# Kernel tuning notes

Measured on AMD Instinct MI355X. Metric: run time of the kernel, lower is better.

The kernel has to match this reference:

```python
import jax, jax.numpy as jnp
import numpy as np

# static config (matches init_kwargs and spatial_shapes input)
SPATIAL = ((100, 100), (50, 50), (25, 25), (13, 13))  # (H, W) per level
D_MODEL, N_HEADS, N_LEVELS, N_POINTS, D_FFN = 256, 8, 4, 4, 1024
D_HEAD = D_MODEL // N_HEADS
LEN_IN = sum(h * w for h, w in SPATIAL)
LEVEL_START = np.cumsum([0] + [h * w for h, w in SPATIAL])[:-1]


def setup_inputs() -> dict:
    key = jax.random.key(0)
    ks = jax.random.split(key, 12)
    N = 2
    f = lambda k, shape, s=0.02: jax.random.normal(k, shape, jnp.float32) * s
    return {
        "src": jax.random.normal(ks[0], (N, LEN_IN, D_MODEL), jnp.float32),
        "pos": jax.random.normal(ks[1], (N, LEN_IN, D_MODEL), jnp.float32),
        "reference_points": jax.random.uniform(ks[2], (N, LEN_IN, N_LEVELS, 2), jnp.float32),
        "spatial_shapes": jnp.asarray(SPATIAL, jnp.int32),
        "level_start_index": jnp.asarray(LEVEL_START, jnp.int32),
        "W_value": f(ks[3], (D_MODEL, D_MODEL)),
        "b_value": jnp.zeros((D_MODEL,), jnp.float32),
        "W_off": f(ks[4], (D_MODEL, N_HEADS * N_LEVELS * N_POINTS * 2)),
        "b_off": f(ks[5], (N_HEADS * N_LEVELS * N_POINTS * 2,), 0.5),
        "W_attn": f(ks[6], (D_MODEL, N_HEADS * N_LEVELS * N_POINTS)),
        "b_attn": jnp.zeros((N_HEADS * N_LEVELS * N_POINTS,), jnp.float32),
        "W_out": f(ks[7], (D_MODEL, D_MODEL)),
        "b_out": jnp.zeros((D_MODEL,), jnp.float32),
        "W1": f(ks[8], (D_MODEL, D_FFN)),
        "b1": jnp.zeros((D_FFN,), jnp.float32),
        "W2": f(ks[9], (D_FFN, D_MODEL)),
        "b2": jnp.zeros((D_MODEL,), jnp.float32),
        "g1": jnp.ones((D_MODEL,), jnp.float32),
        "be1": jnp.zeros((D_MODEL,), jnp.float32),
        "g2": jnp.ones((D_MODEL,), jnp.float32),
        "be2": jnp.zeros((D_MODEL,), jnp.float32),
    }


def _ln(x, g, b, eps=1e-5):
    mu = x.mean(-1, keepdims=True)
    var = ((x - mu) ** 2).mean(-1, keepdims=True)
    return (x - mu) * jax.lax.rsqrt(var + eps) * g + b


def _bilinear(v, loc, H, W):
    # v: [N, heads, H*W, Dh]; loc: [N, Lq, heads, P, 2] normalized to [0,1]
    # replicates F.grid_sample(align_corners=False, padding_mode='zeros') with grid=2*loc-1
    N, Lq, Hh, P, _ = loc.shape
    x = loc[..., 0] * W - 0.5
    y = loc[..., 1] * H - 0.5
    x0 = jnp.floor(x)
    y0 = jnp.floor(y)
    wx1 = x - x0
    wy1 = y - y0
    x0i = x0.astype(jnp.int32)
    y0i = y0.astype(jnp.int32)
    out = jnp.zeros((N, Lq, Hh, P, v.shape[-1]), v.dtype)
    for dy, dx in ((0, 0), (0, 1), (1, 0), (1, 1)):
        xi = x0i + dx
        yi = y0i + dy
        w = (wx1 if dx else 1.0 - wx1) * (wy1 if dy else 1.0 - wy1)
        valid = (xi >= 0) & (xi < W) & (yi >= 0) & (yi < H)
        idx = jnp.clip(yi, 0, H - 1) * W + jnp.clip(xi, 0, W - 1)  # [N,Lq,Hh,P]
        idx = idx.transpose(0, 2, 1, 3).reshape(N, Hh, Lq * P)
        g = jax.vmap(jax.vmap(lambda vm, im: vm[im]))(v, idx)  # [N,Hh,Lq*P,Dh]
        g = g.reshape(N, Hh, Lq, P, -1).transpose(0, 2, 1, 3, 4)
        out = out + (w * valid)[..., None] * g
    return out


def reference(src, pos, reference_points, spatial_shapes, level_start_index,
              W_value, b_value, W_off, b_off, W_attn, b_attn, W_out, b_out,
              W1, b1, W2, b2, g1, be1, g2, be2):
    N, Lq, _ = src.shape
    value = (src @ W_value + b_value).reshape(N, Lq, N_HEADS, D_HEAD)
    q = src + pos  # with_pos_embed
    off = (q @ W_off + b_off).reshape(N, Lq, N_HEADS, N_LEVELS, N_POINTS, 2)
    attn = (q @ W_attn + b_attn).reshape(N, Lq, N_HEADS, N_LEVELS * N_POINTS)
    attn = jax.nn.softmax(attn, axis=-1).reshape(N, Lq, N_HEADS, N_LEVELS, N_POINTS)
    # offset_normalizer = (W, H) per level
    normalizer = jnp.asarray([[w, h] for h, w in SPATIAL], jnp.float32)
    loc = reference_points[:, :, None, :, None, :] + off / normalizer[None, None, None, :, None, :]
    out = jnp.zeros((N, Lq, N_HEADS, D_HEAD), jnp.float32)
    for l, (H, W) in enumerate(SPATIAL):
        s = int(LEVEL_START[l])
        v_l = value[:, s:s + H * W].transpose(0, 2, 1, 3)  # [N, heads, H*W, Dh]
        samp = _bilinear(v_l, loc[:, :, :, l], H, W)       # [N, Lq, heads, P, Dh]
        out = out + jnp.einsum('nqhp,nqhpc->nqhc', attn[:, :, :, l], samp)
    src2 = out.reshape(N, Lq, D_MODEL) @ W_out + b_out
    x = _ln(src + src2, g1, be1)
    ffn = jax.nn.relu(x @ W1 + b1) @ W2 + b2
    return _ln(x + ffn, g2, be2)
```

## Files before the change

### kernel.cpp

```cpp
#include <hip/hip_runtime.h>
#include <hip/hip_bf16.h>
#include <cstdint>

#define D_MODEL   256
#define N_HEADS   8
#define N_LEVELS  4
#define N_POINTS  4
#define D_FFN     1024
#define D_HEAD    32
#define LEN_IN    13294
#define NBATCH    2
#define M_TOK     (NBATCH * LEN_IN)
#define M_PAD     26624

__constant__ int c_lvl_h[4] = {100, 50, 25, 13};
__constant__ int c_lvl_w[4] = {100, 50, 25, 13};
__constant__ int c_lvl_s[4] = {0, 10000, 12500, 13125};

typedef __attribute__((ext_vector_type(8))) __bf16 bf16x8;
typedef __attribute__((ext_vector_type(4))) __bf16 bf16x4;
typedef __attribute__((ext_vector_type(4))) float  f32x4;
typedef __attribute__((ext_vector_type(4))) uint32_t u32x4;

__device__ __forceinline__ float bflo(uint32_t w) { return __uint_as_float(w << 16); }
__device__ __forceinline__ float bfhi(uint32_t w) { return __uint_as_float(w & 0xffff0000u); }

__device__ __forceinline__ void lds_direct16(const void* g, void* l) {
    __builtin_amdgcn_global_load_lds(
        (const __attribute__((address_space(1))) uint32_t*)(uintptr_t)g,
        (__attribute__((address_space(3))) uint32_t*)(uintptr_t)l,
        16, 0, 0);
}

__global__ __launch_bounds__(256) void prep(
    const float* __restrict__ s0, const float* __restrict__ s1, const float* __restrict__ s2,
    const float* __restrict__ s3, const float* __restrict__ s4, const float* __restrict__ s5,
    __bf16* __restrict__ d0, __bf16* __restrict__ d1, __bf16* __restrict__ d2,
    __bf16* __restrict__ d3, __bf16* __restrict__ d4, __bf16* __restrict__ d5,
    const float* __restrict__ b_off, const float* __restrict__ b_attn,
    float* __restrict__ bias_oa,
    const float4* __restrict__ src, const float4* __restrict__ pos,
    bf16x4* __restrict__ sb, bf16x4* __restrict__ qb, int n4)
{
    const int tid = threadIdx.x;
    const int b = blockIdx.x;
    if (b >= 737) {
        const int i = (b - 737) * 256 + tid;
        if (i >= n4) return;
        const float4 s = src[i];
        const float4 p = pos[i];
        bf16x4 sv = { (__bf16)s.x, (__bf16)s.y, (__bf16)s.z, (__bf16)s.w };
        bf16x4 qv = { (__bf16)(s.x + p.x), (__bf16)(s.y + p.y),
                      (__bf16)(s.z + p.z), (__bf16)(s.w + p.w) };
        sb[i] = sv;
        qb[i] = qv;
        return;
    }
    if (b == 736) {
        if (tid < 256) bias_oa[tid] = b_off[tid];
        if (tid < 128) bias_oa[256 + tid] = b_attn[tid];
        return;
    }
    const int tx = tid & 31;
    const int ty = tid >> 5;
    const int starts[7] = {0, 64, 128, 160, 224, 480, 736};
    const int Ks[6] = {256, 256, 256, 256, 256, 1024};
    const int Ns[6] = {256, 256, 128, 256, 1024, 256};
    const float* srcs[6] = {s0, s1, s2, s3, s4, s5};
    __bf16* dsts[6] = {d0, d1, d2, d3, d4, d5};
    int i = 0;
    while (b >= starts[i + 1]) ++i;
    const int t = b - starts[i];
    const int K = Ks[i], N = Ns[i];
    const float* W = srcs[i];
    __bf16* Wt = dsts[i];
    const int ntx = N >> 5;
    const int n0 = (t % ntx) * 32;
    const int k0 = (t / ntx) * 32;

    __shared__ float tl[32][33];
    #pragma unroll
    for (int j = 0; j < 4; ++j)
        tl[ty + j * 8][tx] = W[(size_t)(k0 + ty + j * 8) * N + n0 + tx];
    __syncthreads();
    #pragma unroll
    for (int j = 0; j < 4; ++j)
        Wt[(size_t)(n0 + ty + j * 8) * K + k0 + tx] = (__bf16)tl[tx][ty + j * 8];
}

template <bool RELU, int K, bool HEADMAJOR>
__device__ __forceinline__ void gemm_core(
    const __bf16* __restrict__ A, const __bf16* __restrict__ Bt,
    const float* __restrict__ bias, __bf16* __restrict__ C,
    int M, int N, int bm, int bn)
{
    __shared__ __bf16 smem[17408];
    __bf16* As = smem;
    __bf16* Bs = smem + 8192;

    const int tid  = threadIdx.x;
    const int lane = tid & 63;
    const int wv   = tid >> 6;
    const int wm   = (wv >> 1) * 64;
    const int wn   = (wv & 1) * 64;
    const int srow = lane >> 2;
    const int skc  = (lane & 3) * 8;
    const int fm   = lane & 15;
    const int fko  = (lane >> 4) * 8;

    f32x4 acc[4][4] = {};

    for (int k0 = 0; k0 < K; k0 += 64) {
        #pragma unroll
        for (int p = 0; p < 2; ++p) {
            #pragma unroll
            for (int c = 0; c < 2; ++c) {
                const int r = wv * 32 + c * 16;
                lds_direct16(A  + (size_t)(bm + r + srow) * K + k0 + p * 32 + skc, As + p * 4096 + r * 32);
                lds_direct16(Bt + (size_t)(bn + r + srow) * K + k0 + p * 32 + skc, Bs + p * 4096 + r * 32);
            }
        }
        __syncthreads();

        #pragma unroll
        for (int p = 0; p < 2; ++p) {
            bf16x8 af[4], bfr[4];
            #pragma unroll
            for (int t = 0; t < 4; ++t) {
                af[t]  = *(const bf16x8*)(As + p * 4096 + (wm + t * 16 + fm) * 32 + fko);
                bfr[t] = *(const bf16x8*)(Bs + p * 4096 + (wn + t * 16 + fm) * 32 + fko);
            }
            #pragma unroll
            for (int mt = 0; mt < 4; ++mt)
                #pragma unroll
                for (int nt = 0; nt < 4; ++nt)
                    acc[mt][nt] = __builtin_amdgcn_mfma_f32_16x16x32_bf16(
                        af[mt], bfr[nt], acc[mt][nt], 0, 0, 0);
        }
        __syncthreads();
    }

    const int ecol = lane & 15;
    const int erow = (lane >> 4) * 4;
    #pragma unroll
    for (int nt = 0; nt < 4; ++nt) {
        const int cl = wn + nt * 16 + ecol;
        const float bv = bias[bn + cl];
        #pragma unroll
        for (int mt = 0; mt < 4; ++mt) {
            #pragma unroll
            for (int r = 0; r < 4; ++r) {
                const int rl = wm + mt * 16 + erow + r;
                float v = acc[mt][nt][r] + bv;
                if (RELU) v = fmaxf(v, 0.f);
                smem[rl * 136 + cl] = (__bf16)v;
            }
        }
    }
    __syncthreads();
    #pragma unroll
    for (int rr = 0; rr < 8; ++rr) {
        const int idx = rr * 256 + tid;
        if (HEADMAJOR) {
            const int plane = idx >> 9;
            const int row   = (idx >> 2) & 127;
            const int ch4   = idx & 3;
            if (bm + row < M)
                *(bf16x8*)(C + ((size_t)((bn >> 5) + plane) * M_PAD + (bm + row)) * 32 + ch4 * 8) =
                    *(const bf16x8*)(smem + row * 136 + plane * 32 + ch4 * 8);
        } else {
            const int row = idx >> 4;
            const int ch  = idx & 15;
            if (bm + row < M)
                *(bf16x8*)(C + (size_t)(bm + row) * N + bn + ch * 8) =
                    *(const bf16x8*)(smem + row * 136 + ch * 8);
        }
    }
}

__global__ __launch_bounds__(256) void gemm_front(
    const __bf16* __restrict__ A0, const __bf16* __restrict__ B0,
    const float* __restrict__ bi0, __bf16* __restrict__ C0,
    const __bf16* __restrict__ A1, const __bf16* __restrict__ B1,
    const float* __restrict__ bi1, __bf16* __restrict__ C1, int M)
{
    const int bx = blockIdx.x;
    if (bx < 2)
        gemm_core<false, 256, true>(A0, B0, bi0, C0, M, 256, blockIdx.y * 128, bx * 128);
    else
        gemm_core<false, 256, false>(A1, B1, bi1, C1, M, 384, blockIdx.y * 128, (bx - 2) * 128);
}

__global__ __launch_bounds__(256) void gemm_ffn1(
    const __bf16* __restrict__ A, const __bf16* __restrict__ Bt,
    const float* __restrict__ bias, __bf16* __restrict__ C, int M)
{
    gemm_core<true, 256, false>(A, Bt, bias, C, M, 1024, blockIdx.y * 128, blockIdx.x * 128);
}

template <typename OutT, int K>
__global__ __launch_bounds__(256, 3) void gemm_ln(
    const __bf16* __restrict__ A, const __bf16* __restrict__ Bt,
    const float* __restrict__ bias, const __bf16* __restrict__ res,
    const float* __restrict__ gamma, const float* __restrict__ beta,
    OutT* __restrict__ Cout, int M)
{
    __shared__ __bf16 smem[2][12288];
    __shared__ float lnsum[32][4];
    __shared__ float lnsq[32][4];
    __shared__ float lnstat[32][2];

    const int tid  = threadIdx.x;
    const int lane = tid & 63;
    const int wv   = tid >> 6;
    const int bm   = blockIdx.x * 32;
    const int wn   = wv * 64;
    const int srow = lane >> 2;
    const int skc  = (lane & 3) * 8;
    const int fm   = lane & 15;
    const int fko  = (lane >> 4) * 8;

    f32x4 acc[2][4] = {};

    auto stage = [&](int b, int k0) {
        __bf16* Asw = smem[b] + wv * 1024;
        __bf16* Bsw = smem[b] + 4096;
        lds_direct16(A + (size_t)(bm +  0 + srow) * K + k0 + skc, Asw);
        lds_direct16(A + (size_t)(bm + 16 + srow) * K + k0 + skc, Asw + 512);
        #pragma unroll
        for (int c = 0; c < 4; ++c) {
            const int r = wv * 64 + c * 16;
            lds_direct16(Bt + (size_t)(r + srow) * K + k0 + skc, Bsw + r * 32);
        }
    };
    auto compute = [&](int b) {
        const __bf16* Asw = smem[b] + wv * 1024;
        const __bf16* Bsw = smem[b] + 4096;
        bf16x8 af[2], bfr[4];
        #pragma unroll
        for (int mt = 0; mt < 2; ++mt)
            af[mt] = *(const bf16x8*)(Asw + (mt * 16 + fm) * 32 + fko);
        #pragma unroll
        for (int nt = 0; nt < 4; ++nt)
            bfr[nt] = *(const bf16x8*)(Bsw + (wn + nt * 16 + fm) * 32 + fko);
        #pragma unroll
        for (int mt = 0; mt < 2; ++mt)
            #pragma unroll
            for (int nt = 0; nt < 4; ++nt)
                acc[mt][nt] = __builtin_amdgcn_mfma_f32_16x16x32_bf16(
                    af[mt], bfr[nt], acc[mt][nt], 0, 0, 0);
    };

    stage(0, 0);
    int cur = 0;
    for (int k0 = 32; k0 < K; k0 += 32) {
        stage(cur ^ 1, k0);
        asm volatile("s_waitcnt vmcnt(6)" ::: "memory");
        __builtin_amdgcn_sched_barrier(0);
        compute(cur);
        cur ^= 1;
    }
    asm volatile("s_waitcnt vmcnt(0)" ::: "memory");
    __builtin_amdgcn_sched_barrier(0);
    compute(cur);

    const int ecol = lane & 15;
    const int erow = (lane >> 4) * 4;

    float g4[4], b4[4];
    #pragma unroll
    for (int nt = 0; nt < 4; ++nt) {
        const int col = wn + nt * 16 + ecol;
        g4[nt] = gamma[col];
        b4[nt] = beta[col];
        const float bv = bias[col];
        #pragma unroll
        for (int mt = 0; mt < 2; ++mt) {
            #pragma unroll
            for (int r = 0; r < 4; ++r) {
                const int row = bm + mt * 16 + erow + r;
                acc[mt][nt][r] += bv + (float)res[(size_t)row * 256 + col];
            }
        }
    }

    #pragma unroll
    for (int mt = 0; mt < 2; ++mt) {
        #pragma unroll
        for (int r = 0; r < 4; ++r) {
            float s  = acc[mt][0][r] + acc[mt][1][r] + acc[mt][2][r] + acc[mt][3][r];
            float s2 = acc[mt][0][r] * acc[mt][0][r] + acc[mt][1][r] * acc[mt][1][r]
                     + acc[mt][2][r] * acc[mt][2][r] + acc[mt][3][r] * acc[mt][3][r];
            #pragma unroll
            for (int o = 1; o < 16; o <<= 1) {
                s  += __shfl_xor(s, o);
                s2 += __shfl_xor(s2, o);
            }
            if (ecol == 0) {
                const int rl = mt * 16 + erow + r;
                lnsum[rl][wv] = s;
                lnsq[rl][wv]  = s2;
            }
        }
    }
    __syncthreads();
    if (tid < 32) {
        const float s  = lnsum[tid][0] + lnsum[tid][1] + lnsum[tid][2] + lnsum[tid][3];
        const float s2 = lnsq[tid][0] + lnsq[tid][1] + lnsq[tid][2] + lnsq[tid][3];
        const float mu = s * (1.f / 256.f);
        const float var = s2 * (1.f / 256.f) - mu * mu;
        lnstat[tid][0] = mu;
        lnstat[tid][1] = rsqrtf(var + 1e-5f);
    }
    __syncthreads();

    if constexpr (sizeof(OutT) == 2) {
        __bf16* ct = smem[0];
        #pragma unroll
        for (int mt = 0; mt < 2; ++mt) {
            #pragma unroll
            for (int r = 0; r < 4; ++r) {
                const int rl = mt * 16 + erow + r;
                const float mu = lnstat[rl][0];
                const float rs = lnstat[rl][1];
                #pragma unroll
                for (int nt = 0; nt < 4; ++nt) {
                    const int col = wn + nt * 16 + ecol;
                    ct[rl * 264 + col] = (__bf16)((acc[mt][nt][r] - mu) * rs * g4[nt] + b4[nt]);
                }
            }
        }
        __syncthreads();
        #pragma unroll
        for (int rr = 0; rr < 4; ++rr) {
            const int idx = rr * 256 + tid;
            const int row = idx >> 5;
            const int ch  = idx & 31;
            if (bm + row < M)
                *(bf16x8*)((__bf16*)Cout + (size_t)(bm + row) * 256 + ch * 8) =
                    *(const bf16x8*)(ct + row * 264 + ch * 8);
        }
    } else {
        float* ct = (float*)smem[0];
        #pragma unroll
        for (int hf = 0; hf < 2; ++hf) {
            const int mt = hf;
            #pragma unroll
            for (int r = 0; r < 4; ++r) {
                const int rl   = mt * 16 + erow + r;
                const int rloc = erow + r;
                const float mu = lnstat[rl][0];
                const float rs = lnstat[rl][1];
                #pragma unroll
                for (int nt = 0; nt < 4; ++nt) {
                    const int col = wn + nt * 16 + ecol;
                    ct[rloc * 260 + col] = (acc[mt][nt][r] - mu) * rs * g4[nt] + b4[nt];
                }
            }
            __syncthreads();
            #pragma unroll
            for (int rr = 0; rr < 4; ++rr) {
                const int idx = rr * 256 + tid;
                const int row = idx >> 6;
                const int ch  = idx & 63;
                const int grow = bm + hf * 16 + row;
                if (grow < M) {
                    float4 v = *(const float4*)(ct + row * 260 + ch * 4);
                    *(float4*)((float*)Cout + (size_t)grow * 256 + ch * 4) = v;
                }
            }
            __syncthreads();
        }
    }
}

__global__ __launch_bounds__(256) void msda_sample(
    const __bf16* __restrict__ value,
    const __bf16* __restrict__ oa,
    const float* __restrict__ refp,
    __bf16* __restrict__ out)
{
    __shared__ uint32_t sc[32 * 132];
    __shared__ float sw[32][16];

    const int tid   = threadIdx.x;
    const int blk   = blockIdx.x;
    const int hbase = blockIdx.y * 2;

    if (tid < 32) {
        const int t = tid >> 1;
        const int h = hbase + (tid & 1);
        int row = blk * 16 + t; if (row >= M_TOK) row = M_TOK - 1;
        const __bf16* ap = oa + (size_t)row * 384 + 256 + h * 16;
        const bf16x8 v0 = *(const bf16x8*)ap;
        const bf16x8 v1 = *(const bf16x8*)(ap + 8);
        float e[16];
        #pragma unroll
        for (int i = 0; i < 8; ++i) { e[i] = (float)v0[i]; e[8 + i] = (float)v1[i]; }
        float mx = -1e30f;
        #pragma unroll
        for (int i = 0; i < 16; ++i) mx = fmaxf(mx, e[i]);
        float s = 0.f;
        #pragma unroll
        for (int i = 0; i < 16; ++i) { e[i] = __expf(e[i] - mx); s += e[i]; }
        const float inv = 1.f / s;
        #pragma unroll
        for (int i = 0; i < 16; ++i) sw[tid][i] = e[i] * inv;
    }
    __syncthreads();

    #pragma unroll
    for (int it = 0; it < 2; ++it) {
        const int idx = it * 256 + tid;
        const int t  = idx >> 5;
        const int hl = (idx >> 4) & 1;
        const int lp = idx & 15;
        const int l  = lp >> 2;
        const int h  = hbase + hl;
        int row = blk * 16 + t; if (row >= M_TOK) row = M_TOK - 1;
        const int Ww = c_lvl_w[l];
        const int Hh = c_lvl_h[l];
        const uint32_t opk = *(const uint32_t*)(oa + (size_t)row * 384 + h * 32 + lp * 2);
        const float ox = bflo(opk), oy = bfhi(opk);
        const float rx = refp[((size_t)row * 4 + l) * 2 + 0];
        const float ry = refp[((size_t)row * 4 + l) * 2 + 1];
        const float x = (rx + ox / (float)Ww) * (float)Ww - 0.5f;
        const float y = (ry + oy / (float)Hh) * (float)Hh - 0.5f;
        const float xf = floorf(x), yf = floorf(y);
        const float fx = x - xf,    fy = y - yf;
        const int x0 = (int)xf, y0 = (int)yf;
        const int n  = (row >= LEN_IN) ? 1 : 0;
        const int lvlbase = n * LEN_IN + c_lvl_s[l];
        const float a = sw[t * 2 + hl][lp];
        const int xs = min(max(x0, 0), Ww - 2);
        const int d  = x0 - xs;
        const float wxl = 1.f - fx, wxr = fx;
        const float pw0 = (d == 0) ? wxl : ((d == -1) ? wxr : 0.f);
        const float pw1 = (d == 0) ? wxr : ((d == 1) ? wxl : 0.f);
        uint32_t* p = sc + (t * 2 + hl) * 132 + lp * 8;
        #pragma unroll
        for (int dy = 0; dy < 2; ++dy) {
            const int yi = y0 + dy;
            const int yc = min(max(yi, 0), Hh - 1);
            const bool yv = (yi >= 0) & (yi < Hh);
            const float wy = (dy ? fy : 1.f - fy) * (yv ? a : 0.f);
            const uint32_t boff = (uint32_t)(lvlbase + yc * Ww + xs) * 64u;
            u32x4 pk = { boff, __float_as_uint(pw0 * wy), __float_as_uint(pw1 * wy), 0u };
            *(u32x4*)(p + dy * 4) = pk;
        }
    }
    __syncthreads();

    const int t  = tid >> 4;
    const int hl = (tid >> 3) & 1;
    const int c8 = tid & 7;
    const int h  = hbase + hl;
    const uint32_t* mb = sc + (t * 2 + hl) * 132;
    const char* __restrict__ vpb = (const char*)(value + (size_t)h * (M_PAD * 32));
    const uint32_t lsub = (uint32_t)c8 * 16u;
    const bool hi = (c8 >= 4);
    float acc[8] = {};
    #pragma unroll 8
    for (int qd = 0; qd < 32; ++qd) {
        const u32x4 md = *(const u32x4*)(mb + qd * 4);
        const float w = __uint_as_float(hi ? md.z : md.y);
        const u32x4 v = *(const u32x4*)(vpb + (size_t)(md.x + lsub));
        #pragma unroll
        for (int d2 = 0; d2 < 4; ++d2) {
            acc[2 * d2]     += w * bflo(v[d2]);
            acc[2 * d2 + 1] += w * bfhi(v[d2]);
        }
    }
    #pragma unroll
    for (int j = 0; j < 8; ++j) acc[j] += __shfl_xor(acc[j], 4);
    if (c8 < 4) {
        const int orow = blk * 16 + t;
        if (orow < M_TOK) {
            bf16x8 o;
            #pragma unroll
            for (int j = 0; j < 8; ++j) o[j] = (__bf16)acc[j];
            *(bf16x8*)(out + (size_t)orow * 256 + h * 32 + c8 * 8) = o;
        }
    }
}

extern "C" void kernel_launch(void* const* d_in, const int* in_sizes, int n_in,
                              void* d_out, int out_size, void* d_ws, size_t ws_size,
                              hipStream_t stream)
{
    const float* src     = (const float*)d_in[0];
    const float* pos     = (const float*)d_in[1];
    const float* refp    = (const float*)d_in[2];
    const float* W_value = (const float*)d_in[5];
    const float* b_value = (const float*)d_in[6];
    const float* W_off   = (const float*)d_in[7];
    const float* b_off   = (const float*)d_in[8];
    const float* W_attn  = (const float*)d_in[9];
    const float* b_attn  = (const float*)d_in[10];
    const float* W_out   = (const float*)d_in[11];
    const float* b_out   = (const float*)d_in[12];
    const float* W1      = (const float*)d_in[13];
    const float* b1      = (const float*)d_in[14];
    const float* W2      = (const float*)d_in[15];
    const float* b2      = (const float*)d_in[16];
    const float* g1      = (const float*)d_in[17];
    const float* be1     = (const float*)d_in[18];
    const float* g2      = (const float*)d_in[19];
    const float* be2     = (const float*)d_in[20];
    float* outp = (float*)d_out;

    const int M = M_TOK;
    char* ws = (char*)d_ws;
    const size_t R2 = (size_t)M_PAD * 512;

    __bf16* src_b = (__bf16*)(ws);
    __bf16* q_b   = (__bf16*)(ws + R2);
    __bf16* val_b = (__bf16*)(ws + 2 * R2);
    __bf16* oa    = (__bf16*)(ws + 3 * R2);
    __bf16* samp  = (__bf16*)(ws + 9 * R2 / 2);
    __bf16* x_b   = (__bf16*)(ws + 11 * R2 / 2);
    __bf16* hbuf  = (__bf16*)(ws);
    __bf16* wbase = (__bf16*)(ws + 13 * R2 / 2);
    __bf16* Wt_value = wbase;
    __bf16* Wt_oa    = wbase + 65536;
    __bf16* Wt_out   = wbase + 163840;
    __bf16* Wt1      = wbase + 229376;
    __bf16* Wt2      = wbase + 491520;
    float*  bias_oa  = (float*)(wbase + 753664);

    const dim3 blk(256);
    const int n4 = M * 256 / 4;
    const int gm = M_PAD / 128;

    prep<<<dim3(737 + (n4 + 255) / 256), blk, 0, stream>>>(
        W_value, W_off, W_attn, W_out, W1, W2,
        Wt_value, Wt_oa, Wt_oa + 65536, Wt_out, Wt1, Wt2,
        b_off, b_attn, bias_oa,
        (const float4*)src, (const float4*)pos, (bf16x4*)src_b, (bf16x4*)q_b, n4);

    gemm_front<<<dim3(5, gm), blk, 0, stream>>>(
        src_b, Wt_value, b_value, val_b,
        q_b,   Wt_oa,    bias_oa, oa, M);

    msda_sample<<<dim3((M + 15) / 16, 4), blk, 0, stream>>>(val_b, oa, refp, samp);

    gemm_ln<__bf16, 256><<<dim3(M_PAD / 32), blk, 0, stream>>>(
        samp, Wt_out, b_out, src_b, g1, be1, x_b, M);

    gemm_ffn1<<<dim3(8, gm), blk, 0, stream>>>(x_b, Wt1, b1, hbuf, M);

    gemm_ln<float, 1024><<<dim3(M_PAD / 32), blk, 0, stream>>>(
        hbuf, Wt2, b2, x_b, g2, be2, outp, M);
}
```

Before: 298.2 us.

## Swizzle GEMM block order across XCDs and share A tile in gemm_ln

The front and FFN1 GEMMs now flatten the grid index and remap it so that each XCD (f & 7) handles a contiguous range of M tiles, which should improve L2 reuse of A rows. gemm_ln stops giving each wave its own copy of the A tile and loads a single shared 32x32 A tile, which shrinks shared memory and raises the occupancy hint from 3 to 4 blocks. Synchronisation there changes from per-wave vmcnt waits to block-wide __syncthreads. The risk is that the block barriers and the remap arithmetic add overhead, and the remap assumes a fixed grid shape.

Result: faster. 290.3 us (-2.6%).

```diff
diff --git a/kernel.cpp b/kernel.cpp
--- a/kernel.cpp
+++ b/kernel.cpp
@@ -184,28 +184,38 @@
     const __bf16* __restrict__ A1, const __bf16* __restrict__ B1,
     const float* __restrict__ bi1, __bf16* __restrict__ C1, int M)
 {
-    const int bx = blockIdx.x;
-    if (bx < 2)
-        gemm_core<false, 256, true>(A0, B0, bi0, C0, M, 256, blockIdx.y * 128, bx * 128);
+    const int f   = blockIdx.y * 5 + blockIdx.x;
+    const int xcd = f & 7;
+    const int j   = f >> 3;
+    const int sel = j / 26;
+    const int mm  = j - sel * 26;
+    const int bm  = (xcd * 26 + mm) * 128;
+    if (sel < 2)
+        gemm_core<false, 256, true >(A0, B0, bi0, C0, M, 256, bm, sel * 128);
     else
-        gemm_core<false, 256, false>(A1, B1, bi1, C1, M, 384, blockIdx.y * 128, (bx - 2) * 128);
+        gemm_core<false, 256, false>(A1, B1, bi1, C1, M, 384, bm, (sel - 2) * 128);
 }
 
 __global__ __launch_bounds__(256) void gemm_ffn1(
     const __bf16* __restrict__ A, const __bf16* __restrict__ Bt,
     const float* __restrict__ bias, __bf16* __restrict__ C, int M)
 {
-    gemm_core<true, 256, false>(A, Bt, bias, C, M, 1024, blockIdx.y * 128, blockIdx.x * 128);
+    const int f   = blockIdx.y * 8 + blockIdx.x;
+    const int xcd = f & 7;
+    const int j   = f >> 3;
+    const int nt_ = j / 26;
+    const int mm  = j - nt_ * 26;
+    gemm_core<true, 256, false>(A, Bt, bias, C, M, 1024, (xcd * 26 + mm) * 128, nt_ * 128);
 }
 
 template <typename OutT, int K>
-__global__ __launch_bounds__(256, 3) void gemm_ln(
+__global__ __launch_bounds__(256, 4) void gemm_ln(
     const __bf16* __restrict__ A, const __bf16* __restrict__ Bt,
     const float* __restrict__ bias, const __bf16* __restrict__ res,
     const float* __restrict__ gamma, const float* __restrict__ beta,
     OutT* __restrict__ Cout, int M)
 {
-    __shared__ __bf16 smem[2][12288];
+    __shared__ __bf16 smem[2][9216];
     __shared__ float lnsum[32][4];
     __shared__ float lnsq[32][4];
     __shared__ float lnstat[32][2];
@@ -223,26 +233,27 @@
     f32x4 acc[2][4] = {};
 
     auto stage = [&](int b, int k0) {
-        __bf16* Asw = smem[b] + wv * 1024;
-        __bf16* Bsw = smem[b] + 4096;
-        lds_direct16(A + (size_t)(bm +  0 + srow) * K + k0 + skc, Asw);
-        lds_direct16(A + (size_t)(bm + 16 + srow) * K + k0 + skc, Asw + 512);
+        __bf16* As = smem[b];
+        __bf16* Bs = smem[b] + 1024;
+        if (tid < 128)
+            lds_direct16(A + (size_t)(bm + (tid >> 2)) * K + k0 + (tid & 3) * 8,
+                         As + tid * 8);
         #pragma unroll
         for (int c = 0; c < 4; ++c) {
             const int r = wv * 64 + c * 16;
-            lds_direct16(Bt + (size_t)(r + srow) * K + k0 + skc, Bsw + r * 32);
+            lds_direct16(Bt + (size_t)(r + srow) * K + k0 + skc, Bs + r * 32);
         }
     };
     auto compute = [&](int b) {
-        const __bf16* Asw = smem[b] + wv * 1024;
-        const __bf16* Bsw = smem[b] + 4096;
+        const __bf16* As = smem[b];
+        const __bf16* Bs = smem[b] + 1024;
         bf16x8 af[2], bfr[4];
         #pragma unroll
         for (int mt = 0; mt < 2; ++mt)
-            af[mt] = *(const bf16x8*)(Asw + (mt * 16 + fm) * 32 + fko);
+            af[mt] = *(const bf16x8*)(As + (mt * 16 + fm) * 32 + fko);
         #pragma unroll
         for (int nt = 0; nt < 4; ++nt)
-            bfr[nt] = *(const bf16x8*)(Bsw + (wn + nt * 16 + fm) * 32 + fko);
+            bfr[nt] = *(const bf16x8*)(Bs + (wn + nt * 16 + fm) * 32 + fko);
         #pragma unroll
         for (int mt = 0; mt < 2; ++mt)
             #pragma unroll
@@ -252,16 +263,14 @@
     };
 
     stage(0, 0);
+    __syncthreads();
     int cur = 0;
     for (int k0 = 32; k0 < K; k0 += 32) {
         stage(cur ^ 1, k0);
-        asm volatile("s_waitcnt vmcnt(6)" ::: "memory");
-        __builtin_amdgcn_sched_barrier(0);
         compute(cur);
+        __syncthreads();
         cur ^= 1;
     }
-    asm volatile("s_waitcnt vmcnt(0)" ::: "memory");
-    __builtin_amdgcn_sched_barrier(0);
     compute(cur);
 
     const int ecol = lane & 15;
```
